# Performance work log

Measured on AMD Instinct MI355X. Metric: run time of the kernel, lower is better.

Reference implementation:

```python
import jax, jax.numpy as jnp
import numpy as np

N_E = 1024
E_DIM = 256
BETA = 0.25


def setup_inputs() -> dict:
    key = jax.random.key(0)
    k1, k2 = jax.random.split(key)
    z = jax.random.normal(k1, (16, E_DIM, 64, 64), dtype=jnp.float32)
    # nn.Embedding weight initialized uniform(-1/n_e, 1/n_e)
    codebook = jax.random.uniform(k2, (N_E, E_DIM), dtype=jnp.float32,
                                  minval=-1.0 / N_E, maxval=1.0 / N_E)
    return {"z": z, "codebook": codebook}


def reference(z, codebook):
    B, C, H, W = z.shape
    zp = jnp.transpose(z, (0, 2, 3, 1))              # [B,H,W,C]
    zf = zp.reshape(-1, C)                           # [N, e_dim]
    d = (jnp.sum(zf * zf, axis=1, keepdims=True)
         + jnp.sum(codebook * codebook, axis=1)
         - 2.0 * zf @ codebook.T)                    # [N, n_e]
    idx = jnp.argmin(d, axis=1)                      # [N]
    # one-hot @ codebook == direct gather
    z_q = codebook[idx].reshape(zp.shape)            # [B,H,W,C]

    e_latent_loss = jnp.mean((jax.lax.stop_gradient(z_q) - zp) ** 2)
    q_latent_loss = jnp.mean((z_q - jax.lax.stop_gradient(zp)) ** 2)
    codebook_loss = q_latent_loss + BETA * e_latent_loss

    # straight-through estimator
    z_q_st = zp + jax.lax.stop_gradient(z_q - zp)
    out = jnp.transpose(z_q_st, (0, 3, 1, 2))        # [B,C,H,W]
    indices = idx.reshape(B, 1, H, W)
    return out, codebook_loss, indices
```

## Files before the change

kernel.cpp:

```cpp
#include <hip/hip_runtime.h>

#define NB 16
#define NC 256
#define NH 64
#define NW 64
#define NK 1024
#define HW (NH * NW)
#define NPOS (NB * HW)
#define NOUT (NB * NC * HW)
#define NSLOT 256
#define TP 32

__device__ __forceinline__ float sq_rn(float x) { return __fmul_rn(x, x); }

__device__ __forceinline__ float pairwise_sumsq_256(const float* __restrict__ a,
                                                    int stride) {
    float s_half[2];
#pragma unroll
    for (int h = 0; h < 2; ++h) {
        const float* base = a + (size_t)(h * 128) * stride;
        float r[8];
#pragma unroll
        for (int j = 0; j < 8; ++j) r[j] = sq_rn(base[(size_t)j * stride]);
        for (int i = 8; i < 128; i += 8) {
#pragma unroll
            for (int j = 0; j < 8; ++j)
                r[j] = __fadd_rn(r[j], sq_rn(base[(size_t)(i + j) * stride]));
        }
        s_half[h] = __fadd_rn(
            __fadd_rn(__fadd_rn(r[0], r[1]), __fadd_rn(r[2], r[3])),
            __fadd_rn(__fadd_rn(r[4], r[5]), __fadd_rn(r[6], r[7])));
    }
    return __fadd_rn(s_half[0], s_half[1]);
}

__global__ __launch_bounds__(256) void cnorm_kernel(const float* __restrict__ cb,
                                                    float* __restrict__ cnorm) {
    int k = blockIdx.x * 256 + threadIdx.x;
    if (k < NK) {
        cnorm[k] = pairwise_sumsq_256(cb + (size_t)k * NC, 1);
    }
}

__global__ __launch_bounds__(256) void pack_cb_kernel(const float* __restrict__ cb,
                                                      float* __restrict__ cbT3) {
    const int k = blockIdx.x;
    const int d = threadIdx.x;
    const int it = d >> 2, dl = d & 3;
    const int kb = k >> 7;
    const int q = k & 7;
    const int cgi = (k >> 3) & 15;
    cbT3[(size_t)(((it * 8 + kb) * 128) + q * 16 + cgi) * 4 + dl] =
        cb[(size_t)k * NC + d];
}

__global__ __launch_bounds__(256, 2) void argmin_kernel(const float* __restrict__ z,
                                                        const float* __restrict__ cb,
                                                        const float* __restrict__ cbT3,
                                                        const float* __restrict__ cnorm,
                                                        float* __restrict__ out,
                                                        float* __restrict__ idx_out,
                                                        double* __restrict__ loss_acc) {
    __shared__ float z_lds[256][TP];
    __shared__ float znorm_s[TP];
    __shared__ float red_v[4][TP];
    __shared__ int   red_i[4][TP];

    const int blk = blockIdx.x;
    const int b = blk >> 7;
    const int hw0 = (blk & 127) * TP;
    const int t = threadIdx.x;
    const int lane = t & 63;
    const int wave = t >> 6;
    const int pg = lane >> 4;
    const int cg = lane & 15;

    const float* zg = z + (size_t)b * (NC * HW) + hw0;

#pragma unroll
    for (int i = 0; i < 8; ++i) {
        const int d = i * 32 + (t >> 3);
        const int p = (t & 7) * 4;
        const float4 v = *(const float4*)(zg + (size_t)d * HW + p);
        *(float4*)&z_lds[d][p] = v;
    }
    if (t < TP) znorm_s[t] = pairwise_sumsq_256(zg + t, HW);
    __syncthreads();

    float best[8];
    int bid[8];
#pragma unroll
    for (int i = 0; i < 8; ++i) { best[i] = 3.4e38f; bid[i] = 0; }

#pragma unroll 1
    for (int pass = 0; pass < 2; ++pass) {
        float acc[8][8];
#pragma unroll
        for (int i = 0; i < 8; ++i)
#pragma unroll
            for (int j = 0; j < 8; ++j) acc[i][j] = 0.f;

        const int k0 = wave * 256 + pass * 128 + cg * 8;
        const float* cp3 = cbT3 + (size_t)((wave * 2 + pass) * 512 + cg * 4);

#pragma unroll 1
        for (int it = 0; it < 64; ++it) {
            float4 cbuf[8];
#pragma unroll
            for (int q = 0; q < 8; ++q)
                cbuf[q] = *(const float4*)(cp3 + (size_t)it * 4096 + q * 64);
#pragma unroll
            for (int dl = 0; dl < 4; ++dl) {
                const int d = it * 4 + dl;
                const float4 za = *(const float4*)&z_lds[d][pg * 8];
                const float4 zb = *(const float4*)&z_lds[d][pg * 8 + 4];
                const float zf[8] = {za.x, za.y, za.z, za.w,
                                     zb.x, zb.y, zb.z, zb.w};
#pragma unroll
                for (int i = 0; i < 8; ++i)
#pragma unroll
                    for (int j = 0; j < 8; ++j)
                        acc[i][j] = __fmaf_rn(zf[i],
                                              ((const float*)&cbuf[j])[dl],
                                              acc[i][j]);
            }
        }

        const float4 cn0 = *(const float4*)(cnorm + k0);
        const float4 cn1 = *(const float4*)(cnorm + k0 + 4);
        const float cnf[8] = {cn0.x, cn0.y, cn0.z, cn0.w,
                              cn1.x, cn1.y, cn1.z, cn1.w};
        float znl[8];
#pragma unroll
        for (int i = 0; i < 8; ++i) znl[i] = znorm_s[pg * 8 + i];
#pragma unroll
        for (int j = 0; j < 8; ++j) {
            const int k = k0 + j;
#pragma unroll
            for (int i = 0; i < 8; ++i) {
                const float sc = __fsub_rn(__fadd_rn(znl[i], cnf[j]),
                                           __fmul_rn(2.0f, acc[i][j]));
                if (sc < best[i]) { best[i] = sc; bid[i] = k; }
            }
        }
    }

#pragma unroll
    for (int off = 8; off >= 1; off >>= 1) {
#pragma unroll
        for (int i = 0; i < 8; ++i) {
            const float v = __shfl_down(best[i], off, 64);
            const int d2 = __shfl_down(bid[i], off, 64);
            if (v < best[i] || (v == best[i] && d2 < bid[i])) {
                best[i] = v;
                bid[i] = d2;
            }
        }
    }
    if (cg == 0) {
#pragma unroll
        for (int i = 0; i < 8; ++i) {
            red_v[wave][pg * 8 + i] = best[i];
            red_i[wave][pg * 8 + i] = bid[i];
        }
    }
    __syncthreads();

    if (t < TP) {
        float bv = red_v[0][t];
        int bi = red_i[0][t];
#pragma unroll
        for (int w = 1; w < 4; ++w) {
            const float v = red_v[w][t];
            const int i2 = red_i[w][t];
            if (v < bv || (v == bv && i2 < bi)) { bv = v; bi = i2; }
        }
        idx_out[b * HW + hw0 + t] = (float)bi;
        red_i[0][t] = bi;
    }
    __syncthreads();

    float* outg = out + (size_t)b * (NC * HW) + hw0;
    float lsum = 0.f;
#pragma unroll 1
    for (int r = 0; r < 8; ++r) {
        const int id = r * 256 + t;
        const int c = id >> 3;
        const int p4 = (id & 7) * 4;
        const int i0 = red_i[0][p4];
        const int i1 = red_i[0][p4 + 1];
        const int i2 = red_i[0][p4 + 2];
        const int i3 = red_i[0][p4 + 3];
        float4 o;
        o.x = cb[(size_t)i0 * NC + c];
        o.y = cb[(size_t)i1 * NC + c];
        o.z = cb[(size_t)i2 * NC + c];
        o.w = cb[(size_t)i3 * NC + c];
        *(float4*)(outg + (size_t)c * HW + p4) = o;
        const float4 zv = *(const float4*)&z_lds[c][p4];
        const float d0 = o.x - zv.x;
        const float d1 = o.y - zv.y;
        const float d2 = o.z - zv.z;
        const float d3 = o.w - zv.w;
        lsum += d0 * d0 + d1 * d1 + d2 * d2 + d3 * d3;
    }
#pragma unroll
    for (int off = 32; off > 0; off >>= 1) lsum += __shfl_down(lsum, off, 64);
    if (lane == 0) red_v[wave][0] = lsum;
    __syncthreads();
    if (t == 0) {
        float s = 0.f;
#pragma unroll
        for (int w = 0; w < 4; ++w) s += red_v[w][0];
        atomicAdd(loss_acc + (blk & (NSLOT - 1)), (double)s);
    }
}

__global__ void finalize_kernel(const double* __restrict__ loss_acc,
                                float* __restrict__ out_loss) {
    if (threadIdx.x == 0) {
        double s = 0.0;
        for (int i = 0; i < NSLOT; ++i) s += loss_acc[i];
        *out_loss = (float)(1.25 * s / (double)NOUT);
    }
}

extern "C" void kernel_launch(void* const* d_in, const int* in_sizes, int n_in,
                              void* d_out, int out_size, void* d_ws, size_t ws_size,
                              hipStream_t stream) {
    const float* z = (const float*)d_in[0];
    const float* cb = (const float*)d_in[1];

    float* out = (float*)d_out;
    float* loss_out = out + NOUT;
    float* idx_out = out + NOUT + 1;

    double* loss_acc = (double*)d_ws;
    float* cnorm = (float*)((char*)d_ws + 2048);
    float* cbT3 = (float*)((char*)d_ws + 2048 + 4096);

    hipMemsetAsync(d_ws, 0, 2048, stream);
    cnorm_kernel<<<(NK + 255) / 256, 256, 0, stream>>>(cb, cnorm);
    pack_cb_kernel<<<NK, 256, 0, stream>>>(cb, cbT3);
    argmin_kernel<<<NPOS / TP, 256, 0, stream>>>(z, cb, cbT3, cnorm,
                                                 out, idx_out, loss_acc);
    finalize_kernel<<<1, 64, 0, stream>>>(loss_acc, loss_out);
}
```

Before: 543.6 us.

## Double-buffer codebook loads, compute z norms from LDS, raise occupancy hint

The inner codebook loop now double-buffers its global loads into two register sets, with sched_barrier fences so the load for the next iteration is in flight while the current one computes. The z-norm computation reads from the LDS tile using 64 threads (two halves combined via shuffle) instead of 32 threads doing strided global reads, and a barrier before first use in pass 0 lets it overlap with the first GEMM pass. Launch bounds ask for 3 blocks per SM. The extra buffer adds register pressure against the tighter occupancy target, which may cause spills.

```diff
diff --git a/kernel.cpp b/kernel.cpp
--- a/kernel.cpp
+++ b/kernel.cpp
@@ -54,7 +54,33 @@
         cb[(size_t)k * NC + d];
 }
 
-__global__ __launch_bounds__(256, 2) void argmin_kernel(const float* __restrict__ z,
+__device__ __forceinline__ void load8(float4* __restrict__ buf,
+                                      const float* __restrict__ cp3, int itx) {
+#pragma unroll
+    for (int q = 0; q < 8; ++q)
+        buf[q] = *(const float4*)(cp3 + (size_t)itx * 4096 + q * 64);
+}
+
+__device__ __forceinline__ void compute_it(const float4* __restrict__ cbuf,
+                                           float acc[8][8],
+                                           const float (*z_lds)[TP],
+                                           int it, int pg) {
+#pragma unroll
+    for (int dl = 0; dl < 4; ++dl) {
+        const int d = it * 4 + dl;
+        const float4 za = *(const float4*)&z_lds[d][pg * 8];
+        const float4 zb = *(const float4*)&z_lds[d][pg * 8 + 4];
+        const float zf[8] = {za.x, za.y, za.z, za.w, zb.x, zb.y, zb.z, zb.w};
+#pragma unroll
+        for (int i = 0; i < 8; ++i)
+#pragma unroll
+            for (int j = 0; j < 8; ++j)
+                acc[i][j] = __fmaf_rn(zf[i], ((const float*)&cbuf[j])[dl],
+                                      acc[i][j]);
+    }
+}
+
+__global__ __launch_bounds__(256, 3) void argmin_kernel(const float* __restrict__ z,
                                                         const float* __restrict__ cb,
                                                         const float* __restrict__ cbT3,
                                                         const float* __restrict__ cnorm,
@@ -84,8 +110,26 @@
         const float4 v = *(const float4*)(zg + (size_t)d * HW + p);
         *(float4*)&z_lds[d][p] = v;
     }
-    if (t < TP) znorm_s[t] = pairwise_sumsq_256(zg + t, HW);
-    __syncthreads();
+    __syncthreads();
+
+    if (t < 64) {
+        const int p = t >> 1;
+        const int h = t & 1;
+        const float* base = &z_lds[h * 128][p];
+        float r[8];
+#pragma unroll
+        for (int j = 0; j < 8; ++j) r[j] = sq_rn(base[(size_t)j * TP]);
+        for (int i = 8; i < 128; i += 8) {
+#pragma unroll
+            for (int j = 0; j < 8; ++j)
+                r[j] = __fadd_rn(r[j], sq_rn(base[(size_t)(i + j) * TP]));
+        }
+        const float s = __fadd_rn(
+            __fadd_rn(__fadd_rn(r[0], r[1]), __fadd_rn(r[2], r[3])),
+            __fadd_rn(__fadd_rn(r[4], r[5]), __fadd_rn(r[6], r[7])));
+        const float other = __shfl_down(s, 1, 64);
+        if (h == 0) znorm_s[p] = __fadd_rn(s, other);
+    }
 
     float best[8];
     int bid[8];
@@ -103,29 +147,20 @@
         const int k0 = wave * 256 + pass * 128 + cg * 8;
         const float* cp3 = cbT3 + (size_t)((wave * 2 + pass) * 512 + cg * 4);
 
+        float4 bufA[8], bufB[8];
+        load8(bufA, cp3, 0);
 #pragma unroll 1
-        for (int it = 0; it < 64; ++it) {
-            float4 cbuf[8];
-#pragma unroll
-            for (int q = 0; q < 8; ++q)
-                cbuf[q] = *(const float4*)(cp3 + (size_t)it * 4096 + q * 64);
-#pragma unroll
-            for (int dl = 0; dl < 4; ++dl) {
-                const int d = it * 4 + dl;
-                const float4 za = *(const float4*)&z_lds[d][pg * 8];
-                const float4 zb = *(const float4*)&z_lds[d][pg * 8 + 4];
-                const float zf[8] = {za.x, za.y, za.z, za.w,
-                                     zb.x, zb.y, zb.z, zb.w};
-#pragma unroll
-                for (int i = 0; i < 8; ++i)
-#pragma unroll
-                    for (int j = 0; j < 8; ++j)
-                        acc[i][j] = __fmaf_rn(zf[i],
-                                              ((const float*)&cbuf[j])[dl],
-                                              acc[i][j]);
-            }
-        }
-
+        for (int itp = 0; itp < 32; ++itp) {
+            const int it0 = itp * 2;
+            load8(bufB, cp3, it0 + 1);
+            __builtin_amdgcn_sched_barrier(0);
+            compute_it(bufA, acc, z_lds, it0, pg);
+            if (itp < 31) load8(bufA, cp3, it0 + 2);
+            __builtin_amdgcn_sched_barrier(0);
+            compute_it(bufB, acc, z_lds, it0 + 1, pg);
+        }
+
+        if (pass == 0) __syncthreads();
         const float4 cn0 = *(const float4*)(cnorm + k0);
         const float4 cn1 = *(const float4*)(cnorm + k0 + 4);
         const float cnf[8] = {cn0.x, cn0.y, cn0.z, cn0.w,
```

After: 1.272 ms. +134.0%, slower.
